# Performance work log

Hardware: AMD Instinct MI355X
Metric: run time of the kernel (lower is better)

Reference implementation:

```python
import jax, jax.numpy as jnp
import numpy as np

HEADS = 12
BUCKETS = 256          # position_buckets -> pos_ebd_size (att_span)
MAXPOS = 512           # max_relative_positions
GAMMA = 0.0            # forward() default gamma
LN_EPS = 1e-7


def _make_log_bucket_position(rel, bucket_size, max_position):
    # numpy, host-side constant (shapes are static)
    mid = bucket_size // 2
    sign = np.sign(rel)
    abs_pos = np.where((rel < mid) & (rel > -mid), mid - 1, np.abs(rel)).astype(np.float32)
    log_pos = np.ceil(np.log(abs_pos / mid) / np.log((max_position - 1) / mid) * (mid - 1)) + mid
    return np.where(abs_pos <= mid, rel, (log_pos * sign).astype(np.int64)).astype(np.int64)


def _build_relative_position(q_size, k_size):
    rel = np.arange(q_size)[:, None] - np.arange(k_size)[None, :]
    return _make_log_bucket_position(rel, BUCKETS, MAXPOS)  # [q, k] int64


def _pproc_linear(x, W, b, gamma):
    # pproc: zp * stop_grad(z / zp) with player weights = W + gamma*relu(W)
    z = x @ W.T + b
    pW = W + gamma * jnp.clip(W, 0.0, None)
    pb = b + gamma * jnp.clip(b, 0.0, None)
    zp = x @ pW.T + pb
    return zp * jax.lax.stop_gradient(z / zp)


def setup_inputs() -> dict:
    key = jax.random.key(0)
    ks = jax.random.split(key, 12)
    B, S, H = 4, 1024, 768
    s = 0.02
    return {
        "hidden_states": jax.random.normal(ks[0], (B, S, H), jnp.float32),
        "rel_embeddings": jax.random.normal(ks[1], (2 * BUCKETS, H), jnp.float32),
        "Wq": jax.random.normal(ks[2], (H, H), jnp.float32) * s,
        "bq": jax.random.normal(ks[3], (H,), jnp.float32) * s,
        "Wk": jax.random.normal(ks[4], (H, H), jnp.float32) * s,
        "bk": jax.random.normal(ks[5], (H,), jnp.float32) * s,
        "Wv": jax.random.normal(ks[6], (H, H), jnp.float32) * s,
        "bv": jax.random.normal(ks[7], (H,), jnp.float32) * s,
        "Wo": jax.random.normal(ks[8], (H, H), jnp.float32) * s,
        "bo": jax.random.normal(ks[9], (H,), jnp.float32) * s,
        "ln_w": jnp.ones((H,), jnp.float32),
        "ln_b": jnp.zeros((H,), jnp.float32),
    }


def reference(hidden_states, rel_embeddings, Wq, bq, Wk, bk, Wv, bv, Wo, bo, ln_w, ln_b):
    B, S, H = hidden_states.shape
    d = H // HEADS
    span = BUCKETS  # att_span = pos_ebd_size

    # Q/K/V via pproc dual-layer trick (eval mode, gamma=0 -> plain linear fwd)
    q = _pproc_linear(hidden_states, Wq, bq, GAMMA).reshape(B, S, HEADS, d).transpose(0, 2, 1, 3)
    k = _pproc_linear(hidden_states, Wk, bk, GAMMA).reshape(B, S, HEADS, d).transpose(0, 2, 1, 3)
    v = _pproc_linear(hidden_states, Wv, bv, GAMMA).reshape(B, S, HEADS, d).transpose(0, 2, 1, 3)

    scale_factor = 3.0  # 1 + c2p + p2c
    scale = jnp.sqrt(jnp.float32(d) * scale_factor)
    scores = jnp.einsum("bhsd,bhtd->bhst", q, k) / scale  # [B,H,S,S]

    # disentangled attention bias
    rel = jnp.asarray(_build_relative_position(S, S))  # [S,S] int64 bucketed
    pos_emb = rel_embeddings[: 2 * span]               # [2K, H]
    # share_att_key=True: reuse query/key projections (plain, no pproc)
    pos_k = (pos_emb @ Wk.T + bk).reshape(2 * span, HEADS, d).transpose(1, 0, 2)  # [H,2K,d]
    pos_q = (pos_emb @ Wq.T + bq).reshape(2 * span, HEADS, d).transpose(1, 0, 2)  # [H,2K,d]

    # c2p: gather over bucket axis
    c2p_att = jnp.einsum("bhsd,hkd->bhsk", q, pos_k)                      # [B,H,S,2K]
    c2p_idx = jnp.clip(rel + span, 0, 2 * span - 1)[None, None]           # [1,1,S,S]
    c2p = jnp.take_along_axis(c2p_att, jnp.broadcast_to(c2p_idx, (B, HEADS, S, S)), axis=-1) / scale

    # p2c: gather then transpose
    p2c_att = jnp.einsum("bhtd,hkd->bhtk", k, pos_q)                      # [B,H,S,2K]
    p2c_idx = jnp.clip(-rel + span, 0, 2 * span - 1)[None, None]
    p2c = jnp.take_along_axis(p2c_att, jnp.broadcast_to(p2c_idx, (B, HEADS, S, S)), axis=-1)
    p2c = jnp.swapaxes(p2c, -1, -2) / scale

    scores = scores + c2p + p2c
    probs = jax.lax.stop_gradient(jax.nn.softmax(scores, axis=-1))  # .detach() in original

    ctx = jnp.einsum("bhst,bhtd->bhsd", probs, v).transpose(0, 2, 1, 3).reshape(B, S, H)

    # self_output.pforward: pproc dense + residual + LayerNorm
    out = _pproc_linear(ctx, Wo, bo, GAMMA) + hidden_states
    mu = jnp.mean(out, axis=-1, keepdims=True)
    var = jnp.mean(jnp.square(out - mu), axis=-1, keepdims=True)
    out = ln_w * (out - mu) / jnp.sqrt(var + LN_EPS) + ln_b
    return out, probs
```

## Files before the change

kernel.cpp:

```cpp
#include <hip/hip_runtime.h>

#define BB 4
#define SS 1024
#define HH 768
#define NH 12
#define DD 64
#define SPAN 256
#define TWOSPAN 512
#define NBH (BB * NH)
#define TOT (BB * SS * HH)
#define POSTOT (TWOSPAN * HH)
#define WTOT (HH * HH)
#define QKVLD 2304

typedef unsigned short u16;
typedef __attribute__((ext_vector_type(8))) short bf16x8;
typedef __attribute__((ext_vector_type(4))) float f32x4;

__device__ u16 g_hid[TOT];
__device__ u16 g_rel[POSTOT];
__device__ u16 g_W3[3 * WTOT];
__device__ u16 g_b3[3 * HH];
__device__ u16 g_Wo[WTOT];
__device__ u16 g_bo[HH];
__device__ u16 g_lnw[HH];
__device__ u16 g_lnb[HH];

__device__ u16 g_qkv[(BB * SS) * QKVLD];
__device__ u16 g_posqk[TWOSPAN * 1536];
__device__ u16 g_ctx[TOT];

__device__ u16 g_vt[NBH * DD * SS];
__device__ u16 g_c2p[48 * 1024 * 512];
__device__ u16 g_p2cT[48 * 512 * 1024];
__device__ float g_oproj[TOT];
__device__ int g_relidx[2048];
__device__ int g_isfp32;

__device__ __forceinline__ float b2f(u16 u) {
    union { unsigned int i; float f; } x;
    x.i = ((unsigned int)u) << 16;
    return x.f;
}
__device__ __forceinline__ u16 f2b(float f) {
    union { float f; unsigned int i; } x;
    x.f = f;
    unsigned int r = x.i + 0x7fffu + ((x.i >> 16) & 1u);
    return (u16)(r >> 16);
}

__global__ void detect_dtype(const u16* __restrict__ hid) {
    __shared__ int cnt;
    if (threadIdx.x == 0) cnt = 0;
    __syncthreads();
    const u16 u = hid[threadIdx.x * 2];
    const int e = (u >> 7) & 0xFF;
    if (e >= 130) atomicAdd(&cnt, 1);
    __syncthreads();
    if (threadIdx.x == 0) g_isfp32 = (cnt >= 16) ? 1 : 0;
}

struct Srcs { const void* p[12]; };
#define NCVT (TOT + POSTOT + 4 * WTOT + 6 * HH + 2047)

__device__ __forceinline__ u16 cvt1(const void* p, long long i, int isf) {
    return isf ? f2b(((const float*)p)[i]) : ((const u16*)p)[i];
}

__global__ void fused_convert(Srcs s) {
    long long r = (long long)blockIdx.x * 256 + threadIdx.x;
    const int isf = g_isfp32;
    if (r < TOT) { g_hid[r] = cvt1(s.p[0], r, isf); return; }  r -= TOT;
    if (r < POSTOT) { g_rel[r] = cvt1(s.p[1], r, isf); return; }  r -= POSTOT;
    if (r < WTOT) { g_W3[r] = cvt1(s.p[2], r, isf); return; }  r -= WTOT;
    if (r < WTOT) { g_W3[WTOT + r] = cvt1(s.p[4], r, isf); return; }  r -= WTOT;
    if (r < WTOT) { g_W3[2 * WTOT + r] = cvt1(s.p[6], r, isf); return; }  r -= WTOT;
    if (r < WTOT) { g_Wo[r] = cvt1(s.p[8], r, isf); return; }  r -= WTOT;
    if (r < HH) { g_b3[r] = cvt1(s.p[3], r, isf); return; }  r -= HH;
    if (r < HH) { g_b3[HH + r] = cvt1(s.p[5], r, isf); return; }  r -= HH;
    if (r < HH) { g_b3[2 * HH + r] = cvt1(s.p[7], r, isf); return; }  r -= HH;
    if (r < HH) { g_bo[r] = cvt1(s.p[9], r, isf); return; }  r -= HH;
    if (r < HH) { g_lnw[r] = cvt1(s.p[10], r, isf); return; }  r -= HH;
    if (r < HH) { g_lnb[r] = cvt1(s.p[11], r, isf); return; }  r -= HH;
    if (r < 2047) {
        int delta = (int)r - 1023;
        int ad = delta < 0 ? -delta : delta;
        int bucket;
        if (ad <= 128) {
            bucket = delta;
        } else {
            float num = logf((float)ad / 128.0f);
            double v = (double)num / log(511.0 / 128.0) * 127.0;
            int lp = (int)ceil(v) + 128;
            bucket = (delta > 0) ? lp : -lp;
        }
        int idx = bucket + SPAN;
        idx = idx < 0 ? 0 : (idx > 511 ? 511 : idx);
        g_relidx[r] = idx;
    }
}

__global__ __launch_bounds__(256) void mfma_nt_gemm(
    const u16* __restrict__ A, const u16* __restrict__ B, const u16* __restrict__ bias,
    void* __restrict__ C, int lda, int ldb, int ldc, int K, int c_f32,
    unsigned long long aSb, unsigned long long aSh,
    unsigned long long bSb, unsigned long long bSh,
    unsigned long long cSb, unsigned long long cSh)
{
    const int z = blockIdx.z;
    const int bz = z / NH, hz = z % NH;
    A += (size_t)bz * aSb + (size_t)hz * aSh;
    B += (size_t)bz * bSb + (size_t)hz * bSh;
    const size_t coff = (size_t)bz * cSb + (size_t)hz * cSh;

    const int tid = threadIdx.x;
    const int w  = tid >> 6;
    const int l  = tid & 63;
    const int lr = l & 15;
    const int lk = (l >> 4) << 3;
    const int rr = (l >> 4) << 2;
    const int m0 = blockIdx.y * 128 + (w >> 1) * 64;
    const int n0 = blockIdx.x * 128 + (w & 1) * 64;

    f32x4 acc[4][4] = {};
    for (int k0 = 0; k0 < K; k0 += 32) {
        bf16x8 af[4], bfr[4];
        #pragma unroll
        for (int m = 0; m < 4; ++m)
            af[m] = *(const bf16x8*)(A + (size_t)(m0 + m * 16 + lr) * lda + k0 + lk);
        #pragma unroll
        for (int n = 0; n < 4; ++n)
            bfr[n] = *(const bf16x8*)(B + (size_t)(n0 + n * 16 + lr) * ldb + k0 + lk);
        #pragma unroll
        for (int m = 0; m < 4; ++m)
            #pragma unroll
            for (int n = 0; n < 4; ++n)
                acc[m][n] = __builtin_amdgcn_mfma_f32_16x16x32_bf16(af[m], bfr[n], acc[m][n], 0, 0, 0);
    }

    #pragma unroll
    for (int m = 0; m < 4; ++m) {
        #pragma unroll
        for (int n = 0; n < 4; ++n) {
            const int col = n0 + n * 16 + lr;
            const float bv = bias ? b2f(bias[col]) : 0.f;
            #pragma unroll
            for (int r = 0; r < 4; ++r) {
                const int row = m0 + m * 16 + rr + r;
                const float v = acc[m][n][r] + bv;
                if (c_f32) ((float*)C)[coff + (size_t)row * ldc + col] = v;
                else       ((u16*)C)[coff + (size_t)row * ldc + col]  = f2b(v);
            }
        }
    }
}

__global__ void vtrans_kernel() {
    const int i = blockIdx.x * 256 + threadIdx.x;
    const int d = i & 63;
    const int t = (i >> 6) & 1023;
    const int z = i >> 16;
    const int b = z / NH, h = z % NH;
    g_vt[((size_t)z * DD + d) * SS + t] =
        g_qkv[((size_t)(b * SS + t)) * QKVLD + 2 * HH + h * DD + d];
}

__global__ __launch_bounds__(256, 3) void attn_fused_kernel(void* __restrict__ dout, int has_probs)
{
    const int nblk = blockIdx.x;
    const int xcd  = nblk & 7;
    const int jj0  = nblk >> 3;
    const int z    = xcd * 6 + (jj0 >> 6);
    const int s0   = (jj0 & 63) * 16;
    const int b    = z / NH, h = z % NH;
    const int tid  = threadIdx.x;
    const int w    = tid >> 6;
    const int l    = tid & 63;
    const int lr   = l & 15;
    const int hi   = l >> 4;
    const int lk8  = hi << 3;
    const int rr   = hi << 2;

    __shared__ __align__(16) char smem[32768];
    __shared__ int   relw[1040];
    __shared__ float redm[4][16];
    __shared__ float reds[4][16];

    for (int i = tid; i < 1040; i += 256) relw[i] = g_relidx[s0 + i];

    const u16* __restrict__ qb = g_qkv + ((size_t)(b * SS + s0)) * QKVLD + h * DD;
    const u16* __restrict__ kb = g_qkv + ((size_t)(b * SS)) * QKVLD + HH + h * DD;
    const bf16x8 aq0 = *(const bf16x8*)(qb + (size_t)lr * QKVLD + lk8);
    const bf16x8 aq1 = *(const bf16x8*)(qb + (size_t)lr * QKVLD + 32 + lk8);

    const int t0 = w * 256;
    f32x4 acc[16];
    #pragma unroll
    for (int nn = 0; nn < 16; ++nn) {
        const u16* kp = kb + (size_t)(t0 + nn * 16 + lr) * QKVLD;
        const bf16x8 bk0 = *(const bf16x8*)(kp + lk8);
        const bf16x8 bk1 = *(const bf16x8*)(kp + 32 + lk8);
        f32x4 a = {};
        a = __builtin_amdgcn_mfma_f32_16x16x32_bf16(aq0, bk0, a, 0, 0, 0);
        a = __builtin_amdgcn_mfma_f32_16x16x32_bf16(aq1, bk1, a, 0, 0, 0);
        acc[nn] = a;
    }
    __syncthreads();

    const float rscale = 0.07216878364870323f;
    const u16* __restrict__ c2pb = g_c2p  + ((size_t)z * SS + s0) * TWOSPAN;
    const u16* __restrict__ p2cb = g_p2cT + (size_t)z * TWOSPAN * SS;
    #pragma unroll
    for (int nn = 0; nn < 16; ++nn) {
        const int t = t0 + nn * 16 + lr;
        #pragma unroll
        for (int r = 0; r < 4; ++r) {
            const int srow = rr + r;
            const int j = relw[srow - t + 1023];
            acc[nn][r] = (acc[nn][r] + b2f(c2pb[srow * TWOSPAN + j])
                                     + b2f(p2cb[(size_t)j * SS + t])) * rscale;
        }
    }

    float mr[4];
    #pragma unroll
    for (int r = 0; r < 4; ++r) {
        float m = acc[0][r];
        #pragma unroll
        for (int nn = 1; nn < 16; ++nn) m = fmaxf(m, acc[nn][r]);
        #pragma unroll
        for (int off = 1; off < 16; off <<= 1) m = fmaxf(m, __shfl_xor(m, off));
        mr[r] = m;
    }
    if (lr == 0) {
        #pragma unroll
        for (int r = 0; r < 4; ++r) redm[w][rr + r] = mr[r];
    }
    __syncthreads();
    #pragma unroll
    for (int r = 0; r < 4; ++r) {
        const int srow = rr + r;
        mr[r] = fmaxf(fmaxf(redm[0][srow], redm[1][srow]),
                      fmaxf(redm[2][srow], redm[3][srow]));
    }

    float sr[4] = {0.f, 0.f, 0.f, 0.f};
    #pragma unroll
    for (int nn = 0; nn < 16; ++nn)
        #pragma unroll
        for (int r = 0; r < 4; ++r) {
            const float e = __expf(acc[nn][r] - mr[r]);
            acc[nn][r] = e;
            sr[r] += e;
        }
    #pragma unroll
    for (int r = 0; r < 4; ++r)
        #pragma unroll
        for (int off = 1; off < 16; off <<= 1) sr[r] += __shfl_xor(sr[r], off);
    if (lr == 0) {
        #pragma unroll
        for (int r = 0; r < 4; ++r) reds[w][rr + r] = sr[r];
    }
    __syncthreads();
    float inv[4];
    #pragma unroll
    for (int r = 0; r < 4; ++r) {
        const int srow = rr + r;
        inv[r] = 1.0f / (reds[0][srow] + reds[1][srow] + reds[2][srow] + reds[3][srow]);
    }

    const int isf = g_isfp32;
    #pragma unroll
    for (int nn = 0; nn < 16; ++nn) {
        const int t = t0 + nn * 16 + lr;
        #pragma unroll
        for (int r = 0; r < 4; ++r) {
            const int srow = rr + r;
            const float pv = acc[nn][r] * inv[r];
            const u16 pb = f2b(pv);
            *(u16*)(smem + (srow * 2048 + ((((t >> 3) ^ (srow & 7)) << 4) | ((t & 7) << 1)))) = pb;
            if (has_probs) {
                const size_t base = (size_t)TOT + ((size_t)z * SS + (s0 + srow)) * SS + t;
                if (isf) ((float*)dout)[base] = pv;
                else     ((u16*)dout)[base]   = pb;
            }
        }
    }
    __syncthreads();

    const u16* __restrict__ VT = g_vt + (size_t)z * DD * SS;
    f32x4 cacc[4] = {};
    #pragma unroll
    for (int ks = 0; ks < 8; ++ks) {
        const int kt = t0 + ks * 32;
        const int tA = kt + lk8;
        const bf16x8 pa = *(const bf16x8*)(smem + (lr * 2048 + ((((tA >> 3) ^ (lr & 7)) << 4))));
        #pragma unroll
        for (int nn = 0; nn < 4; ++nn) {
            const bf16x8 bv = *(const bf16x8*)(VT + (size_t)(nn * 16 + lr) * SS + kt + lk8);
            cacc[nn] = __builtin_amdgcn_mfma_f32_16x16x32_bf16(pa, bv, cacc[nn], 0, 0, 0);
        }
    }
    __syncthreads();

    float* ctxp = (float*)smem;
    #pragma unroll
    for (int nn = 0; nn < 4; ++nn)
        #pragma unroll
        for (int r = 0; r < 4; ++r) {
            const int srow = rr + r;
            const int d = nn * 16 + lr;
            ctxp[w * 1024 + srow * 64 + (d ^ ((srow & 3) << 4))] = cacc[nn][r];
        }
    __syncthreads();

    #pragma unroll
    for (int it = 0; it < 4; ++it) {
        const int idx = it * 256 + tid;
        const int srow = idx >> 6;
        const int d = idx & 63;
        const int dd = d ^ ((srow & 3) << 4);
        const float rsum = ctxp[srow * 64 + dd] + ctxp[1024 + srow * 64 + dd]
                         + ctxp[2048 + srow * 64 + dd] + ctxp[3072 + srow * 64 + dd];
        g_ctx[((size_t)(b * SS + s0 + srow)) * HH + h * DD + d] = f2b(rsum);
    }
}

__global__ __launch_bounds__(256) void ln_kernel(void* __restrict__ dout)
{
    const int row = blockIdx.x;
    const int tid = threadIdx.x;
    __shared__ float os[HH];
    __shared__ float red[4];

    for (int c = tid; c < HH; c += 256)
        os[c] = g_oproj[(size_t)row * HH + c] + b2f(g_hid[(size_t)row * HH + c]);
    __syncthreads();

    float sum = 0.f;
    for (int c = tid; c < HH; c += 256) sum += os[c];
    #pragma unroll
    for (int off = 32; off > 0; off >>= 1) sum += __shfl_down(sum, off);
    if ((tid & 63) == 0) red[tid >> 6] = sum;
    __syncthreads();
    if (tid == 0) red[0] = red[0] + red[1] + red[2] + red[3];
    __syncthreads();
    const float mu = red[0] * (1.0f / HH);
    __syncthreads();

    float vs = 0.f;
    for (int c = tid; c < HH; c += 256) {
        const float dd0 = os[c] - mu;
        vs += dd0 * dd0;
    }
    #pragma unroll
    for (int off = 32; off > 0; off >>= 1) vs += __shfl_down(vs, off);
    if ((tid & 63) == 0) red[tid >> 6] = vs;
    __syncthreads();
    if (tid == 0) red[0] = red[0] + red[1] + red[2] + red[3];
    __syncthreads();
    const float var = red[0] * (1.0f / HH);
    const float rstd = 1.0f / sqrtf(var + 1e-7f);

    const int isf = g_isfp32;
    for (int c = tid; c < HH; c += 256) {
        const float o = b2f(g_lnw[c]) * (os[c] - mu) * rstd + b2f(g_lnb[c]);
        if (isf) ((float*)dout)[(size_t)row * HH + c] = o;
        else     ((u16*)dout)[(size_t)row * HH + c]   = f2b(o);
    }
}

extern "C" void kernel_launch(void* const* d_in, const int* in_sizes, int n_in,
                              void* d_out, int out_size, void* d_ws, size_t ws_size,
                              hipStream_t stream) {
    detect_dtype<<<1, 256, 0, stream>>>((const u16*)d_in[0]);

    Srcs s;
    for (int i = 0; i < 12; ++i) s.p[i] = d_in[i];
    fused_convert<<<(NCVT + 255) / 256, 256, 0, stream>>>(s);

    void* p;
    u16 *p_hid, *p_rel, *p_W3, *p_b3, *p_Wo, *p_bo, *p_qkv, *p_posqk, *p_ctx;
    u16 *p_c2p, *p_p2cT;
    float *p_oproj;
    hipGetSymbolAddress(&p, HIP_SYMBOL(g_hid));   p_hid   = (u16*)p;
    hipGetSymbolAddress(&p, HIP_SYMBOL(g_rel));   p_rel   = (u16*)p;
    hipGetSymbolAddress(&p, HIP_SYMBOL(g_W3));    p_W3    = (u16*)p;
    hipGetSymbolAddress(&p, HIP_SYMBOL(g_b3));    p_b3    = (u16*)p;
    hipGetSymbolAddress(&p, HIP_SYMBOL(g_Wo));    p_Wo    = (u16*)p;
    hipGetSymbolAddress(&p, HIP_SYMBOL(g_bo));    p_bo    = (u16*)p;
    hipGetSymbolAddress(&p, HIP_SYMBOL(g_qkv));   p_qkv   = (u16*)p;
    hipGetSymbolAddress(&p, HIP_SYMBOL(g_posqk)); p_posqk = (u16*)p;
    hipGetSymbolAddress(&p, HIP_SYMBOL(g_ctx));   p_ctx   = (u16*)p;
    hipGetSymbolAddress(&p, HIP_SYMBOL(g_c2p));   p_c2p   = (u16*)p;
    hipGetSymbolAddress(&p, HIP_SYMBOL(g_p2cT));  p_p2cT  = (u16*)p;
    hipGetSymbolAddress(&p, HIP_SYMBOL(g_oproj)); p_oproj = (float*)p;

    const int M = BB * SS;
    const unsigned long long Z = 0ull;

    mfma_nt_gemm<<<dim3(QKVLD / 128, M / 128, 1), 256, 0, stream>>>(
        p_hid, p_W3, p_b3, p_qkv, HH, HH, QKVLD, HH, 0, Z, Z, Z, Z, Z, Z);
    mfma_nt_gemm<<<dim3(1536 / 128, TWOSPAN / 128, 1), 256, 0, stream>>>(
        p_rel, p_W3, p_b3, p_posqk, HH, HH, 1536, HH, 0, Z, Z, Z, Z, Z, Z);

    mfma_nt_gemm<<<dim3(TWOSPAN / 128, SS / 128, NBH), 256, 0, stream>>>(
        p_qkv, p_posqk + HH, (const u16*)nullptr, p_c2p, QKVLD, 1536, TWOSPAN, DD, 0,
        (unsigned long long)SS * QKVLD, (unsigned long long)DD,
        Z,                              (unsigned long long)DD,
        (unsigned long long)NH * SS * TWOSPAN, (unsigned long long)SS * TWOSPAN);
    mfma_nt_gemm<<<dim3(SS / 128, TWOSPAN / 128, NBH), 256, 0, stream>>>(
        p_posqk, p_qkv + HH, (const u16*)nullptr, p_p2cT, 1536, QKVLD, SS, DD, 0,
        Z,                               (unsigned long long)DD,
        (unsigned long long)SS * QKVLD,  (unsigned long long)DD,
        (unsigned long long)NH * TWOSPAN * SS, (unsigned long long)TWOSPAN * SS);

    vtrans_kernel<<<(NBH * DD * SS) / 256, 256, 0, stream>>>();

    const long long need = (long long)TOT + (long long)BB * NH * SS * SS;
    const int has_probs = ((long long)out_size >= need) ? 1 : 0;
    attn_fused_kernel<<<NBH * (SS / 16), 256, 0, stream>>>(d_out, has_probs);

    mfma_nt_gemm<<<dim3(HH / 128, M / 128, 1), 256, 0, stream>>>(
        p_ctx, p_Wo, p_bo, p_oproj, HH, HH, HH, HH, 1, Z, Z, Z, Z, Z, Z);

    ln_kernel<<<BB * SS, 256, 0, stream>>>(d_out);
}
```

Before: 669.2 us.

## Stage GEMM tiles in LDS via direct global-to-LDS loads

Measured after the change: 623.4 us. -6.8%, faster.

```diff
diff --git a/kernel.cpp b/kernel.cpp
--- a/kernel.cpp
+++ b/kernel.cpp
@@ -47,6 +47,12 @@
     x.f = f;
     unsigned int r = x.i + 0x7fffu + ((x.i >> 16) & 1u);
     return (u16)(r >> 16);
+}
+
+typedef const __attribute__((address_space(1))) unsigned int gas_uint;
+typedef __attribute__((address_space(3))) unsigned int las_uint;
+__device__ __forceinline__ void gl2lds16(const u16* gp, u16* lp) {
+    __builtin_amdgcn_global_load_lds((gas_uint*)gp, (las_uint*)lp, 16, 0, 0);
 }
 
 __global__ void detect_dtype(const u16* __restrict__ hid) {
@@ -113,40 +119,60 @@
     B += (size_t)bz * bSb + (size_t)hz * bSh;
     const size_t coff = (size_t)bz * cSb + (size_t)hz * cSh;
 
+    __shared__ u16 As[128 * 64];
+    __shared__ u16 Bs[128 * 64];
+
     const int tid = threadIdx.x;
     const int w  = tid >> 6;
     const int l  = tid & 63;
     const int lr = l & 15;
-    const int lk = (l >> 4) << 3;
-    const int rr = (l >> 4) << 2;
-    const int m0 = blockIdx.y * 128 + (w >> 1) * 64;
-    const int n0 = blockIdx.x * 128 + (w & 1) * 64;
+    const int hi = l >> 4;
+    const int rr = hi << 2;
+    const int m0 = blockIdx.y * 128;
+    const int n0 = blockIdx.x * 128;
+    const int wm = (w >> 1) * 64;
+    const int wn = (w & 1) * 64;
+    const int srow = l >> 3;
+    const int scol = (l & 7) * 8;
 
     f32x4 acc[4][4] = {};
-    for (int k0 = 0; k0 < K; k0 += 32) {
-        bf16x8 af[4], bfr[4];
-        #pragma unroll
-        for (int m = 0; m < 4; ++m)
-            af[m] = *(const bf16x8*)(A + (size_t)(m0 + m * 16 + lr) * lda + k0 + lk);
-        #pragma unroll
-        for (int n = 0; n < 4; ++n)
-            bfr[n] = *(const bf16x8*)(B + (size_t)(n0 + n * 16 + lr) * ldb + k0 + lk);
-        #pragma unroll
-        for (int m = 0; m < 4; ++m)
+    for (int k0 = 0; k0 < K; k0 += 64) {
+        #pragma unroll
+        for (int ii = 0; ii < 4; ++ii) {
+            const int ch = w * 4 + ii;
+            const int r  = ch * 8 + srow;
+            gl2lds16(A + (size_t)(m0 + r) * lda + k0 + scol, &As[ch * 512]);
+            gl2lds16(B + (size_t)(n0 + r) * ldb + k0 + scol, &Bs[ch * 512]);
+        }
+        __syncthreads();
+
+        #pragma unroll
+        for (int kk = 0; kk < 2; ++kk) {
+            bf16x8 af[4], bfr[4];
+            #pragma unroll
+            for (int m = 0; m < 4; ++m)
+                af[m] = *(const bf16x8*)&As[(wm + m * 16 + lr) * 64 + kk * 32 + hi * 8];
             #pragma unroll
             for (int n = 0; n < 4; ++n)
-                acc[m][n] = __builtin_amdgcn_mfma_f32_16x16x32_bf16(af[m], bfr[n], acc[m][n], 0, 0, 0);
+                bfr[n] = *(const bf16x8*)&Bs[(wn + n * 16 + lr) * 64 + kk * 32 + hi * 8];
+            #pragma unroll
+            for (int m = 0; m < 4; ++m)
+                #pragma unroll
+                for (int n = 0; n < 4; ++n)
+                    acc[m][n] = __builtin_amdgcn_mfma_f32_16x16x32_bf16(af[m], bfr[n], acc[m][n], 0, 0, 0);
+        }
+        __syncthreads();
     }
 
     #pragma unroll
     for (int m = 0; m < 4; ++m) {
         #pragma unroll
         for (int n = 0; n < 4; ++n) {
-            const int col = n0 + n * 16 + lr;
+            const int col = n0 + wn + n * 16 + lr;
             const float bv = bias ? b2f(bias[col]) : 0.f;
             #pragma unroll
             for (int r = 0; r < 4; ++r) {
-                const int row = m0 + m * 16 + rr + r;
+                const int row = m0 + wm + m * 16 + rr + r;
                 const float v = acc[m][n][r] + bv;
                 if (c_f32) ((float*)C)[coff + (size_t)row * ldc + col] = v;
                 else       ((u16*)C)[coff + (size_t)row * ldc + col]  = f2b(v);
@@ -383,18 +409,18 @@
     u16 *p_hid, *p_rel, *p_W3, *p_b3, *p_Wo, *p_bo, *p_qkv, *p_posqk, *p_ctx;
     u16 *p_c2p, *p_p2cT;
     float *p_oproj;
-    hipGetSymbolAddress(&p, HIP_SYMBOL(g_hid));   p_hid   = (u16*)p;
-    hipGetSymbolAddress(&p, HIP_SYMBOL(g_rel));   p_rel   = (u16*)p;
-    hipGetSymbolAddress(&p, HIP_SYMBOL(g_W3));    p_W3    = (u16*)p;
-    hipGetSymbolAddress(&p, HIP_SYMBOL(g_b3));    p_b3    = (u16*)p;
-    hipGetSymbolAddress(&p, HIP_SYMBOL(g_Wo));    p_Wo    = (u16*)p;
-    hipGetSymbolAddress(&p, HIP_SYMBOL(g_bo));    p_bo    = (u16*)p;
-    hipGetSymbolAddress(&p, HIP_SYMBOL(g_qkv));   p_qkv   = (u16*)p;
-    hipGetSymbolAddress(&p, HIP_SYMBOL(g_posqk)); p_posqk = (u16*)p;
-    hipGetSymbolAddress(&p, HIP_SYMBOL(g_ctx));   p_ctx   = (u16*)p;
-    hipGetSymbolAddress(&p, HIP_SYMBOL(g_c2p));   p_c2p   = (u16*)p;
-    hipGetSymbolAddress(&p, HIP_SYMBOL(g_p2cT));  p_p2cT  = (u16*)p;
-    hipGetSymbolAddress(&p, HIP_SYMBOL(g_oproj)); p_oproj = (float*)p;
+    (void)hipGetSymbolAddress(&p, HIP_SYMBOL(g_hid));   p_hid   = (u16*)p;
+    (void)hipGetSymbolAddress(&p, HIP_SYMBOL(g_rel));   p_rel   = (u16*)p;
+    (void)hipGetSymbolAddress(&p, HIP_SYMBOL(g_W3));    p_W3    = (u16*)p;
+    (void)hipGetSymbolAddress(&p, HIP_SYMBOL(g_b3));    p_b3    = (u16*)p;
+    (void)hipGetSymbolAddress(&p, HIP_SYMBOL(g_Wo));    p_Wo    = (u16*)p;
+    (void)hipGetSymbolAddress(&p, HIP_SYMBOL(g_bo));    p_bo    = (u16*)p;
+    (void)hipGetSymbolAddress(&p, HIP_SYMBOL(g_qkv));   p_qkv   = (u16*)p;
+    (void)hipGetSymbolAddress(&p, HIP_SYMBOL(g_posqk)); p_posqk = (u16*)p;
+    (void)hipGetSymbolAddress(&p, HIP_SYMBOL(g_ctx));   p_ctx   = (u16*)p;
+    (void)hipGetSymbolAddress(&p, HIP_SYMBOL(g_c2p));   p_c2p   = (u16*)p;
+    (void)hipGetSymbolAddress(&p, HIP_SYMBOL(g_p2cT));  p_p2cT  = (u16*)p;
+    (void)hipGetSymbolAddress(&p, HIP_SYMBOL(g_oproj)); p_oproj = (float*)p;
 
     const int M = BB * SS;
     const unsigned long long Z = 0ull;
```
